# Optimization experiments

Hardware: AMD Instinct MI355X
Metric: run time of the kernel (lower is better)

## Reference

```python
import jax, jax.numpy as jnp
import numpy as np

N = 100000      # nodes
E = 1600000     # edges (avg degree 16)
DIN = 128
DOUT = 128


def setup_inputs() -> dict:
    key = jax.random.key(0)
    k1, k2, k3, k4 = jax.random.split(key, 4)
    x = jax.random.normal(k1, (N, DIN), dtype=jnp.float32)
    edge_index = jax.random.randint(k2, (2, E), 0, N, dtype=jnp.int64)
    # guarantee every node appears at least once as a source row so that
    # degree > 0 everywhere (1/sqrt(0) would be inf, as in the torch code)
    row = edge_index[0].at[:N].set(jnp.arange(N, dtype=jnp.int64))
    edge_index = jnp.stack([row, edge_index[1]])
    W = jax.random.normal(k3, (DOUT, DIN), dtype=jnp.float32) / np.sqrt(DIN)
    b = jax.random.normal(k4, (DOUT,), dtype=jnp.float32) * 0.01
    return {"x": x, "edge_index": edge_index, "W": W, "b": b}


def reference(x, edge_index, W, b):
    # Math identical to: A = dense(add_self_loops(edge_index));
    # D = 1/sqrt(degree(edge_index[0]))  (degree WITHOUT self-loops);
    # out = (D_i * A_ij * D_j) @ (x W^T + b)
    row, col = edge_index[0], edge_index[1]
    deg = jax.ops.segment_sum(jnp.ones(row.shape[0], x.dtype), row, num_segments=N)
    d = jax.lax.rsqrt(deg)                      # [N]
    h = x @ W.T + b                             # [N, DOUT]
    # edge contributions: out[r] += D[r] * D[c] * h[c]  (duplicate edges sum, as to_dense does)
    agg = jax.ops.segment_sum(d[col][:, None] * h[col], row, num_segments=N)
    # self-loop term added for every node: D[i]^2 * h[i]
    out = d[:, None] * agg + (d * d)[:, None] * h
    return out
```

## Files before the change

kernel.cpp:

```cpp
#include <hip/hip_runtime.h>

#define D 128
#define BROWS 1024
#define CAP 17408
#define CHUNK 2048

typedef __attribute__((ext_vector_type(8))) short bf16x8;
typedef __attribute__((ext_vector_type(4))) float f32x4;

__device__ inline unsigned short f2bf(float f) {
    unsigned u = __float_as_uint(f);
    u += 0x7FFFu + ((u >> 16) & 1u);
    return (unsigned short)(u >> 16);
}
__device__ inline float bf2f(unsigned short h) {
    return __uint_as_float((unsigned)h << 16);
}
__device__ inline float bflo(unsigned u) { return __uint_as_float(u << 16); }
__device__ inline float bfhi(unsigned u) { return __uint_as_float(u & 0xFFFF0000u); }

__global__ __launch_bounds__(256) void k_bin(const int* __restrict__ row,
                                             const int* __restrict__ col,
                                             int E, int* __restrict__ gcur,
                                             unsigned* __restrict__ ebuf) {
    __shared__ int lhist[128];
    __shared__ int sc[128];
    __shared__ int gbase[128];
    __shared__ unsigned sstage[CHUNK];
    __shared__ int sdest[CHUNK];
    int t = threadIdx.x;
    int base = blockIdx.x * CHUNK;
    if (t < 128) lhist[t] = 0;
    __syncthreads();
    int b[8], p[8]; unsigned pk[8];
    #pragma unroll
    for (int i = 0; i < 8; ++i) {
        int idx = base + i * 256 + t;
        if (idx < E) {
            int r = row[idx], c = col[idx];
            b[i] = r >> 10;
            pk[i] = ((unsigned)(r & (BROWS - 1)) << 17) | (unsigned)c;
            p[i] = atomicAdd(&lhist[b[i]], 1);
        } else b[i] = -1;
    }
    __syncthreads();
    if (t < 64) {
        int a0 = lhist[2 * t], a1 = lhist[2 * t + 1];
        int s = a0 + a1;
        int incl = s;
        #pragma unroll
        for (int m = 1; m < 64; m <<= 1) {
            int tmp = __shfl_up(incl, m);
            if (t >= m) incl += tmp;
        }
        int excl = incl - s;
        sc[2 * t] = excl;
        sc[2 * t + 1] = excl + a0;
        if (a0 > 0) gbase[2 * t] = atomicAdd(&gcur[2 * t], a0);
        if (a1 > 0) gbase[2 * t + 1] = atomicAdd(&gcur[2 * t + 1], a1);
    }
    __syncthreads();
    #pragma unroll
    for (int i = 0; i < 8; ++i) {
        if (b[i] >= 0) {
            int lidx = sc[b[i]] + p[i];
            int rel = gbase[b[i]] + p[i];
            sstage[lidx] = pk[i];
            sdest[lidx] = (rel < CAP) ? (b[i] * CAP + rel) : -1;
        }
    }
    __syncthreads();
    int total = sc[127] + lhist[127];
    for (int i = t; i < total; i += 256) {
        int d = sdest[i];
        if (d >= 0) ebuf[d] = sstage[i];
    }
}

__global__ __launch_bounds__(1024) void k_group(const int* __restrict__ gcur,
                                                const unsigned* __restrict__ ebuf,
                                                int N, int NBK,
                                                float* __restrict__ dvals,
                                                int* __restrict__ rptr,
                                                int* __restrict__ csr_col) {
    __shared__ unsigned sebuf[CAP];
    __shared__ int lhist[1024];
    __shared__ int wtot[16];
    __shared__ int woff[16];
    __shared__ int sebase;
    int bkt = blockIdx.x, t = threadIdx.x;
    int cnt = gcur[bkt]; if (cnt > CAP) cnt = CAP;
    if (t < 64) {
        int acc = 0;
        for (int i = t; i < bkt; i += 64) {
            int g = gcur[i];
            acc += (g > CAP) ? CAP : g;
        }
        #pragma unroll
        for (int m = 1; m < 64; m <<= 1) acc += __shfl_xor(acc, m);
        if (t == 0) sebase = acc;
    }
    lhist[t] = 0;
    __syncthreads();
    const unsigned* ep = ebuf + (size_t)bkt * CAP;
    for (int i = t; i < cnt; i += 1024) {
        unsigned e = ep[i];
        sebuf[i] = e;
        atomicAdd(&lhist[e >> 17], 1);
    }
    __syncthreads();
    int v = lhist[t];
    int lane = t & 63, wv = t >> 6;
    int incl = v;
    #pragma unroll
    for (int m = 1; m < 64; m <<= 1) {
        int tmp = __shfl_up(incl, m);
        if (lane >= m) incl += tmp;
    }
    if (lane == 63) wtot[wv] = incl;
    __syncthreads();
    if (t < 16) {
        int w = wtot[t];
        int wincl = w;
        #pragma unroll
        for (int m = 1; m < 16; m <<= 1) {
            int tmp = __shfl_up(wincl, m);
            if (t >= m) wincl += tmp;
        }
        woff[t] = wincl - w;
    }
    __syncthreads();
    int excl = woff[wv] + incl - v;
    int ebase = sebase;
    int r = (bkt << 10) + t;
    if (r < N) {
        rptr[r] = ebase + excl;
        dvals[r] = rsqrtf((float)v);
    }
    if (bkt == NBK - 1 && t == 0) rptr[N] = ebase + cnt;
    lhist[t] = excl;
    __syncthreads();
    for (int i = t; i < cnt; i += 1024) {
        unsigned e = sebuf[i];
        int rr = (int)(e >> 17);
        int p = atomicAdd(&lhist[rr], 1);
        csr_col[ebase + p] = (int)(e & 0x1FFFFu);
    }
}

__global__ void k_cast(const float* __restrict__ x, const float* __restrict__ dvals,
                       unsigned short* __restrict__ xs, int total4) {
    int i = blockIdx.x * blockDim.x + threadIdx.x;
    if (i >= total4) return;
    float4 v = ((const float4*)x)[i];
    float d = dvals[i >> 5];
    ushort4 o = make_ushort4(f2bf(d * v.x), f2bf(d * v.y), f2bf(d * v.z), f2bf(d * v.w));
    ((ushort4*)xs)[i] = o;
}

#define ACC8(v) do { \
    a[0] += bflo((v).x); a[1] += bfhi((v).x); \
    a[2] += bflo((v).y); a[3] += bfhi((v).y); \
    a[4] += bflo((v).z); a[5] += bfhi((v).z); \
    a[6] += bflo((v).w); a[7] += bfhi((v).w); } while (0)

__global__ __launch_bounds__(256) void k_rows(const unsigned short* __restrict__ xs,
                                              const int* __restrict__ rptr,
                                              const int* __restrict__ csr_col,
                                              const float* __restrict__ dvals,
                                              float* __restrict__ ssum,
                                              float* __restrict__ y, int N) {
    int wid = (blockIdx.x * blockDim.x + threadIdx.x) >> 6;
    if (wid >= N) return;
    int lane = threadIdx.x & 63;
    int grp = lane >> 4, sl = lane & 15;
    int s = rptr[wid];
    int n = rptr[wid + 1] - s;
    const uint4* xsv = (const uint4*)xs;

    int ccreg = (lane < n) ? csr_col[s + lane] : 0;
    float sd = (lane < n) ? dvals[ccreg] : 0.f;
    uint4 vself = make_uint4(0, 0, 0, 0);
    if (grp == 0) vself = xsv[wid * 16 + sl];

    float a[8] = {0.f, 0.f, 0.f, 0.f, 0.f, 0.f, 0.f, 0.f};
    int nf = (n < 64) ? n : 64;
    for (int k0 = 0; k0 < nf; k0 += 16) {
        int i0 = k0 + grp, i1 = i0 + 4, i2 = i0 + 8, i3 = i0 + 12;
        int cc0 = __shfl(ccreg, i0), cc1 = __shfl(ccreg, i1);
        int cc2 = __shfl(ccreg, i2), cc3 = __shfl(ccreg, i3);
        bool p0 = i0 < nf, p1 = i1 < nf, p2 = i2 < nf, p3 = i3 < nf;
        uint4 v0, v1, v2, v3;
        if (p0) v0 = xsv[cc0 * 16 + sl];
        if (p1) v1 = xsv[cc1 * 16 + sl];
        if (p2) v2 = xsv[cc2 * 16 + sl];
        if (p3) v3 = xsv[cc3 * 16 + sl];
        if (p0) ACC8(v0);
        if (p1) ACC8(v1);
        if (p2) ACC8(v2);
        if (p3) ACC8(v3);
    }
    if (__builtin_expect(n > 64, 0)) {
        for (int idx = 64 + grp; idx < n; idx += 4) {
            int cc = csr_col[s + idx];
            uint4 v = xsv[cc * 16 + sl];
            ACC8(v);
        }
        for (int idx = 64 + lane; idx < n; idx += 64)
            sd += dvals[csr_col[s + idx]];
    }
    if (grp == 0) ACC8(vself);

    #pragma unroll
    for (int j = 0; j < 8; ++j) {
        a[j] += __shfl_xor(a[j], 16);
        a[j] += __shfl_xor(a[j], 32);
    }
    #pragma unroll
    for (int m = 1; m < 64; m <<= 1) sd += __shfl_xor(sd, m);

    float dr = dvals[wid];
    if (grp < 2) {
        float4 o = (grp == 0) ? make_float4(a[0], a[1], a[2], a[3])
                              : make_float4(a[4], a[5], a[6], a[7]);
        o.x *= dr; o.y *= dr; o.z *= dr; o.w *= dr;
        ((float4*)(y + (size_t)wid * D))[sl * 2 + grp] = o;
    }
    if (lane == 0) ssum[wid] = dr * (dr + sd);
}

#define LDSW 136

__global__ __launch_bounds__(256, 2) void k_gemm(const float* __restrict__ W,
                                                 const float* __restrict__ b,
                                                 const float* __restrict__ ssum,
                                                 float* yo, int N) {
    __shared__ unsigned short Whi[128 * LDSW];
    __shared__ unsigned short Wlo[128 * LDSW];
    __shared__ float bs[D];
    int t = threadIdx.x;
    #pragma unroll
    for (int i = 0; i < 16; ++i) {
        int idx4 = i * 256 + t;
        float4 w4 = ((const float4*)W)[idx4];
        int r = idx4 >> 5;
        int c = (idx4 & 31) * 4;
        unsigned short h0 = f2bf(w4.x), h1 = f2bf(w4.y), h2 = f2bf(w4.z), h3 = f2bf(w4.w);
        unsigned short l0 = f2bf(w4.x - bf2f(h0));
        unsigned short l1 = f2bf(w4.y - bf2f(h1));
        unsigned short l2 = f2bf(w4.z - bf2f(h2));
        unsigned short l3 = f2bf(w4.w - bf2f(h3));
        ushort4* ph = (ushort4*)&Whi[r * LDSW + c];
        ushort4* pl = (ushort4*)&Wlo[r * LDSW + c];
        *ph = make_ushort4(h0, h1, h2, h3);
        *pl = make_ushort4(l0, l1, l2, l3);
    }
    if (t < D) bs[t] = b[t];
    __syncthreads();

    int wave = t >> 6, lane = t & 63;
    int quad = lane >> 4, mrow = lane & 15;
    int row_base = blockIdx.x * 128 + wave * 32;

    bf16x8 Ahi[2][4], Alo[2][4];
    #pragma unroll
    for (int s = 0; s < 2; ++s) {
        int grow = row_base + s * 16 + mrow;
        bool ok = grow < N;
        const float* yrow = yo + (size_t)(ok ? grow : 0) * D;
        #pragma unroll
        for (int kk = 0; kk < 4; ++kk) {
            int k0 = kk * 32 + quad * 8;
            float4 f0 = ok ? ((const float4*)(yrow + k0))[0] : make_float4(0, 0, 0, 0);
            float4 f1 = ok ? ((const float4*)(yrow + k0))[1] : make_float4(0, 0, 0, 0);
            float fv[8] = {f0.x, f0.y, f0.z, f0.w, f1.x, f1.y, f1.z, f1.w};
            #pragma unroll
            for (int j = 0; j < 8; ++j) {
                unsigned short h = f2bf(fv[j]);
                Ahi[s][kk][j] = (short)h;
                Alo[s][kk][j] = (short)f2bf(fv[j] - bf2f(h));
            }
        }
    }

    f32x4 acc[2][8];
    #pragma unroll
    for (int s = 0; s < 2; ++s)
        #pragma unroll
        for (int ct = 0; ct < 8; ++ct)
            acc[s][ct] = (f32x4){0.f, 0.f, 0.f, 0.f};

    #pragma unroll
    for (int ct = 0; ct < 8; ++ct) {
        int wrow = ct * 16 + mrow;
        #pragma unroll
        for (int kk = 0; kk < 4; ++kk) {
            int off = wrow * LDSW + kk * 32 + quad * 8;
            bf16x8 Bhi = *(const bf16x8*)&Whi[off];
            bf16x8 Blo = *(const bf16x8*)&Wlo[off];
            #pragma unroll
            for (int s = 0; s < 2; ++s) {
                acc[s][ct] = __builtin_amdgcn_mfma_f32_16x16x32_bf16(Ahi[s][kk], Bhi, acc[s][ct], 0, 0, 0);
                acc[s][ct] = __builtin_amdgcn_mfma_f32_16x16x32_bf16(Alo[s][kk], Bhi, acc[s][ct], 0, 0, 0);
                acc[s][ct] = __builtin_amdgcn_mfma_f32_16x16x32_bf16(Ahi[s][kk], Blo, acc[s][ct], 0, 0, 0);
            }
        }
    }

    #pragma unroll
    for (int s = 0; s < 2; ++s) {
        #pragma unroll
        for (int r = 0; r < 4; ++r) {
            int grow = row_base + s * 16 + quad * 4 + r;
            if (grow < N) {
                float sv = ssum[grow];
                #pragma unroll
                for (int ct = 0; ct < 8; ++ct) {
                    int col = ct * 16 + mrow;
                    yo[(size_t)grow * D + col] = acc[s][ct][r] + sv * bs[col];
                }
            }
        }
    }
}

extern "C" void kernel_launch(void* const* d_in, const int* in_sizes, int n_in,
                              void* d_out, int out_size, void* d_ws, size_t ws_size,
                              hipStream_t stream) {
    const float* x  = (const float*)d_in[0];
    const int*   ei = (const int*)d_in[1];
    const float* W  = (const float*)d_in[2];
    const float* b  = (const float*)d_in[3];
    float* out = (float*)d_out;
    int N = in_sizes[0] / D;
    int E = in_sizes[1] / 2;
    int NBK = (N + BROWS - 1) / BROWS;
    int NCH = (E + CHUNK - 1) / CHUNK;

    int*      gcur    = (int*)d_ws;
    int*      rptr    = gcur + 128;
    float*    dvals   = (float*)(rptr + N + 1);
    float*    ssum    = dvals + N;
    int*      csr_col = (int*)(ssum + N);
    unsigned* ebuf    = (unsigned*)(csr_col + E);
    uintptr_t xs_addr = (uintptr_t)(ebuf + (size_t)NBK * CAP);
    xs_addr = (xs_addr + 15) & ~(uintptr_t)15;
    unsigned short* xs = (unsigned short*)xs_addr;

    hipMemsetAsync(gcur, 0, 128 * sizeof(int), stream);
    k_bin<<<NCH, 256, 0, stream>>>(ei, ei + E, E, gcur, ebuf);
    k_group<<<NBK, 1024, 0, stream>>>(gcur, ebuf, N, NBK, dvals, rptr, csr_col);
    k_cast<<<(N * (D / 4) + 255) / 256, 256, 0, stream>>>(x, dvals, xs, N * (D / 4));
    k_rows<<<(N + 3) / 4, 256, 0, stream>>>(xs, rptr, csr_col, dvals, ssum, out, N);
    k_gemm<<<(N + 127) / 128, 256, 0, stream>>>(W, b, ssum, out, N);
}
```

Before: 276.6 us.

## Fuse row aggregation with GEMM and use finer-grained edge bucketing

Merges the gather-aggregate kernel and the split-bf16 MFMA GEMM into one kernel. Each 1024-thread block aggregates 16 rows into LDS as hi/lo bf16 and immediately multiplies them by W, so the fp32 intermediate is no longer written to and re-read from global memory and a launch is dropped. Bucketing now uses 512-row buckets with larger chunks, and a zeroed sentinel row of xs lets the aggregation load without predication. In exchange, each block reloads and converts W from global/L2, only half the waves do the GEMM, and there are more, smaller grouping blocks.

```diff
diff --git a/kernel.cpp b/kernel.cpp
--- a/kernel.cpp
+++ b/kernel.cpp
@@ -1,9 +1,11 @@
 #include <hip/hip_runtime.h>
 
 #define D 128
-#define BROWS 1024
-#define CAP 17408
-#define CHUNK 2048
+#define BROWS 512
+#define LOGB 9
+#define NBMAX 256
+#define CAP 9216
+#define CHUNK 4096
 
 typedef __attribute__((ext_vector_type(8))) short bf16x8;
 typedef __attribute__((ext_vector_type(4))) float f32x4;
@@ -19,34 +21,34 @@
 __device__ inline float bflo(unsigned u) { return __uint_as_float(u << 16); }
 __device__ inline float bfhi(unsigned u) { return __uint_as_float(u & 0xFFFF0000u); }
 
-__global__ __launch_bounds__(256) void k_bin(const int* __restrict__ row,
+__global__ __launch_bounds__(512) void k_bin(const int* __restrict__ row,
                                              const int* __restrict__ col,
                                              int E, int* __restrict__ gcur,
                                              unsigned* __restrict__ ebuf) {
-    __shared__ int lhist[128];
-    __shared__ int sc[128];
-    __shared__ int gbase[128];
+    __shared__ int lhist[NBMAX];
+    __shared__ int sc[NBMAX];
+    __shared__ int gbase[NBMAX];
     __shared__ unsigned sstage[CHUNK];
     __shared__ int sdest[CHUNK];
     int t = threadIdx.x;
     int base = blockIdx.x * CHUNK;
-    if (t < 128) lhist[t] = 0;
+    if (t < NBMAX) lhist[t] = 0;
     __syncthreads();
     int b[8], p[8]; unsigned pk[8];
     #pragma unroll
     for (int i = 0; i < 8; ++i) {
-        int idx = base + i * 256 + t;
+        int idx = base + i * 512 + t;
         if (idx < E) {
             int r = row[idx], c = col[idx];
-            b[i] = r >> 10;
+            b[i] = r >> LOGB;
             pk[i] = ((unsigned)(r & (BROWS - 1)) << 17) | (unsigned)c;
             p[i] = atomicAdd(&lhist[b[i]], 1);
         } else b[i] = -1;
     }
     __syncthreads();
     if (t < 64) {
-        int a0 = lhist[2 * t], a1 = lhist[2 * t + 1];
-        int s = a0 + a1;
+        int a0 = lhist[4*t], a1 = lhist[4*t+1], a2 = lhist[4*t+2], a3 = lhist[4*t+3];
+        int s = a0 + a1 + a2 + a3;
         int incl = s;
         #pragma unroll
         for (int m = 1; m < 64; m <<= 1) {
@@ -54,10 +56,12 @@
             if (t >= m) incl += tmp;
         }
         int excl = incl - s;
-        sc[2 * t] = excl;
-        sc[2 * t + 1] = excl + a0;
-        if (a0 > 0) gbase[2 * t] = atomicAdd(&gcur[2 * t], a0);
-        if (a1 > 0) gbase[2 * t + 1] = atomicAdd(&gcur[2 * t + 1], a1);
+        sc[4*t] = excl; sc[4*t+1] = excl + a0;
+        sc[4*t+2] = excl + a0 + a1; sc[4*t+3] = excl + a0 + a1 + a2;
+        if (a0 > 0) gbase[4*t]   = atomicAdd(&gcur[4*t],   a0);
+        if (a1 > 0) gbase[4*t+1] = atomicAdd(&gcur[4*t+1], a1);
+        if (a2 > 0) gbase[4*t+2] = atomicAdd(&gcur[4*t+2], a2);
+        if (a3 > 0) gbase[4*t+3] = atomicAdd(&gcur[4*t+3], a3);
     }
     __syncthreads();
     #pragma unroll
@@ -70,8 +74,8 @@
         }
     }
     __syncthreads();
-    int total = sc[127] + lhist[127];
-    for (int i = t; i < total; i += 256) {
+    int total = sc[NBMAX - 1] + lhist[NBMAX - 1];
+    for (int i = t; i < total; i += 512) {
         int d = sdest[i];
         if (d >= 0) ebuf[d] = sstage[i];
     }
@@ -84,9 +88,9 @@
                                                 int* __restrict__ rptr,
                                                 int* __restrict__ csr_col) {
     __shared__ unsigned sebuf[CAP];
-    __shared__ int lhist[1024];
-    __shared__ int wtot[16];
-    __shared__ int woff[16];
+    __shared__ int lhist[BROWS];
+    __shared__ int wtot[8];
+    __shared__ int woff[8];
     __shared__ int sebase;
     int bkt = blockIdx.x, t = threadIdx.x;
     int cnt = gcur[bkt]; if (cnt > CAP) cnt = CAP;
@@ -100,7 +104,7 @@
         for (int m = 1; m < 64; m <<= 1) acc += __shfl_xor(acc, m);
         if (t == 0) sebase = acc;
     }
-    lhist[t] = 0;
+    if (t < BROWS) lhist[t] = 0;
     __syncthreads();
     const unsigned* ep = ebuf + (size_t)bkt * CAP;
     for (int i = t; i < cnt; i += 1024) {
@@ -109,36 +113,41 @@
         atomicAdd(&lhist[e >> 17], 1);
     }
     __syncthreads();
-    int v = lhist[t];
     int lane = t & 63, wv = t >> 6;
-    int incl = v;
-    #pragma unroll
-    for (int m = 1; m < 64; m <<= 1) {
-        int tmp = __shfl_up(incl, m);
-        if (lane >= m) incl += tmp;
-    }
-    if (lane == 63) wtot[wv] = incl;
-    __syncthreads();
-    if (t < 16) {
+    int v = 0, incl = 0;
+    if (t < BROWS) {
+        v = lhist[t];
+        incl = v;
+        #pragma unroll
+        for (int m = 1; m < 64; m <<= 1) {
+            int tmp = __shfl_up(incl, m);
+            if (lane >= m) incl += tmp;
+        }
+        if (lane == 63) wtot[wv] = incl;
+    }
+    __syncthreads();
+    if (t < 8) {
         int w = wtot[t];
         int wincl = w;
         #pragma unroll
-        for (int m = 1; m < 16; m <<= 1) {
+        for (int m = 1; m < 8; m <<= 1) {
             int tmp = __shfl_up(wincl, m);
             if (t >= m) wincl += tmp;
         }
         woff[t] = wincl - w;
     }
     __syncthreads();
-    int excl = woff[wv] + incl - v;
     int ebase = sebase;
-    int r = (bkt << 10) + t;
-    if (r < N) {
-        rptr[r] = ebase + excl;
-        dvals[r] = rsqrtf((float)v);
+    if (t < BROWS) {
+        int excl = woff[wv] + incl - v;
+        int r = (bkt << LOGB) + t;
+        if (r < N) {
+            rptr[r] = ebase + excl;
+            dvals[r] = rsqrtf((float)v);
+        }
+        lhist[t] = excl;
     }
     if (bkt == NBK - 1 && t == 0) rptr[N] = ebase + cnt;
-    lhist[t] = excl;
     __syncthreads();
     for (int i = t; i < cnt; i += 1024) {
         unsigned e = sebuf[i];
@@ -164,53 +173,72 @@
     a[4] += bflo((v).z); a[5] += bfhi((v).z); \
     a[6] += bflo((v).w); a[7] += bfhi((v).w); } while (0)
 
-__global__ __launch_bounds__(256) void k_rows(const unsigned short* __restrict__ xs,
-                                              const int* __restrict__ rptr,
-                                              const int* __restrict__ csr_col,
-                                              const float* __restrict__ dvals,
-                                              float* __restrict__ ssum,
-                                              float* __restrict__ y, int N) {
-    int wid = (blockIdx.x * blockDim.x + threadIdx.x) >> 6;
-    if (wid >= N) return;
-    int lane = threadIdx.x & 63;
-    int grp = lane >> 4, sl = lane & 15;
-    int s = rptr[wid];
-    int n = rptr[wid + 1] - s;
+#define YW 136
+
+__global__ __launch_bounds__(1024, 8) void k_fg(const unsigned short* __restrict__ xs,
+                                                const int* __restrict__ rptr,
+                                                const int* __restrict__ csr_col,
+                                                const float* __restrict__ dvals,
+                                                const float* __restrict__ W,
+                                                const float* __restrict__ b,
+                                                float* __restrict__ out, int N) {
+    __shared__ unsigned short yhi[16][YW];
+    __shared__ unsigned short ylo[16][YW];
+    __shared__ float sval[16];
+    int t = threadIdx.x;
+    int w = t >> 6, lane = t & 63, grp = lane >> 4, sl = lane & 15;
+    int r = blockIdx.x * 16 + w;
     const uint4* xsv = (const uint4*)xs;
 
-    int ccreg = (lane < n) ? csr_col[s + lane] : 0;
-    float sd = (lane < n) ? dvals[ccreg] : 0.f;
-    uint4 vself = make_uint4(0, 0, 0, 0);
-    if (grp == 0) vself = xsv[wid * 16 + sl];
-
     float a[8] = {0.f, 0.f, 0.f, 0.f, 0.f, 0.f, 0.f, 0.f};
-    int nf = (n < 64) ? n : 64;
-    for (int k0 = 0; k0 < nf; k0 += 16) {
-        int i0 = k0 + grp, i1 = i0 + 4, i2 = i0 + 8, i3 = i0 + 12;
-        int cc0 = __shfl(ccreg, i0), cc1 = __shfl(ccreg, i1);
-        int cc2 = __shfl(ccreg, i2), cc3 = __shfl(ccreg, i3);
-        bool p0 = i0 < nf, p1 = i1 < nf, p2 = i2 < nf, p3 = i3 < nf;
-        uint4 v0, v1, v2, v3;
-        if (p0) v0 = xsv[cc0 * 16 + sl];
-        if (p1) v1 = xsv[cc1 * 16 + sl];
-        if (p2) v2 = xsv[cc2 * 16 + sl];
-        if (p3) v3 = xsv[cc3 * 16 + sl];
-        if (p0) ACC8(v0);
-        if (p1) ACC8(v1);
-        if (p2) ACC8(v2);
-        if (p3) ACC8(v3);
-    }
-    if (__builtin_expect(n > 64, 0)) {
-        for (int idx = 64 + grp; idx < n; idx += 4) {
-            int cc = csr_col[s + idx];
-            uint4 v = xsv[cc * 16 + sl];
-            ACC8(v);
-        }
-        for (int idx = 64 + lane; idx < n; idx += 64)
-            sd += dvals[csr_col[s + idx]];
-    }
-    if (grp == 0) ACC8(vself);
-
+    float sd = 0.f;
+    if (r < N) {
+        int sbeg = rptr[r];
+        int n = rptr[r + 1] - sbeg;
+        int cc0 = (lane < n) ? csr_col[sbeg + lane] : -1;
+        int ccreg = (cc0 >= 0) ? cc0 : N;
+        sd = (cc0 >= 0) ? dvals[cc0] : 0.f;
+        uint4 vs = make_uint4(0, 0, 0, 0);
+        if (grp == 0) vs = xsv[(size_t)r * 16 + sl];
+        int nf = (n < 64) ? n : 64;
+        if (nf <= 16) {
+            int c0 = __shfl(ccreg, grp),     c1 = __shfl(ccreg, grp + 4);
+            int c2 = __shfl(ccreg, grp + 8), c3 = __shfl(ccreg, grp + 12);
+            uint4 v0 = xsv[(size_t)c0 * 16 + sl];
+            uint4 v1 = xsv[(size_t)c1 * 16 + sl];
+            uint4 v2 = xsv[(size_t)c2 * 16 + sl];
+            uint4 v3 = xsv[(size_t)c3 * 16 + sl];
+            ACC8(v0); ACC8(v1); ACC8(v2); ACC8(v3);
+        } else {
+            for (int k0 = 0; k0 < nf; k0 += 32) {
+                int i0 = k0 + grp;
+                int c0 = __shfl(ccreg, i0),      c1 = __shfl(ccreg, i0 + 4);
+                int c2 = __shfl(ccreg, i0 + 8),  c3 = __shfl(ccreg, i0 + 12);
+                int c4 = __shfl(ccreg, i0 + 16), c5 = __shfl(ccreg, i0 + 20);
+                int c6 = __shfl(ccreg, i0 + 24), c7 = __shfl(ccreg, i0 + 28);
+                uint4 v0 = xsv[(size_t)c0 * 16 + sl];
+                uint4 v1 = xsv[(size_t)c1 * 16 + sl];
+                uint4 v2 = xsv[(size_t)c2 * 16 + sl];
+                uint4 v3 = xsv[(size_t)c3 * 16 + sl];
+                uint4 v4 = xsv[(size_t)c4 * 16 + sl];
+                uint4 v5 = xsv[(size_t)c5 * 16 + sl];
+                uint4 v6 = xsv[(size_t)c6 * 16 + sl];
+                uint4 v7 = xsv[(size_t)c7 * 16 + sl];
+                ACC8(v0); ACC8(v1); ACC8(v2); ACC8(v3);
+                ACC8(v4); ACC8(v5); ACC8(v6); ACC8(v7);
+            }
+        }
+        if (__builtin_expect(n > 64, 0)) {
+            for (int idx = 64 + grp; idx < n; idx += 4) {
+                int cc = csr_col[sbeg + idx];
+                uint4 v = xsv[(size_t)cc * 16 + sl];
+                ACC8(v);
+            }
+            for (int idx = 64 + lane; idx < n; idx += 64)
+                sd += dvals[csr_col[sbeg + idx]];
+        }
+        if (grp == 0) ACC8(vs);
+    }
     #pragma unroll
     for (int j = 0; j < 8; ++j) {
         a[j] += __shfl_xor(a[j], 16);
@@ -219,107 +247,59 @@
     #pragma unroll
     for (int m = 1; m < 64; m <<= 1) sd += __shfl_xor(sd, m);
 
-    float dr = dvals[wid];
-    if (grp < 2) {
-        float4 o = (grp == 0) ? make_float4(a[0], a[1], a[2], a[3])
-                              : make_float4(a[4], a[5], a[6], a[7]);
-        o.x *= dr; o.y *= dr; o.z *= dr; o.w *= dr;
-        ((float4*)(y + (size_t)wid * D))[sl * 2 + grp] = o;
-    }
-    if (lane == 0) ssum[wid] = dr * (dr + sd);
-}
-
-#define LDSW 136
-
-__global__ __launch_bounds__(256, 2) void k_gemm(const float* __restrict__ W,
-                                                 const float* __restrict__ b,
-                                                 const float* __restrict__ ssum,
-                                                 float* yo, int N) {
-    __shared__ unsigned short Whi[128 * LDSW];
-    __shared__ unsigned short Wlo[128 * LDSW];
-    __shared__ float bs[D];
-    int t = threadIdx.x;
-    #pragma unroll
-    for (int i = 0; i < 16; ++i) {
-        int idx4 = i * 256 + t;
-        float4 w4 = ((const float4*)W)[idx4];
-        int r = idx4 >> 5;
-        int c = (idx4 & 31) * 4;
-        unsigned short h0 = f2bf(w4.x), h1 = f2bf(w4.y), h2 = f2bf(w4.z), h3 = f2bf(w4.w);
-        unsigned short l0 = f2bf(w4.x - bf2f(h0));
-        unsigned short l1 = f2bf(w4.y - bf2f(h1));
-        unsigned short l2 = f2bf(w4.z - bf2f(h2));
-        unsigned short l3 = f2bf(w4.w - bf2f(h3));
-        ushort4* ph = (ushort4*)&Whi[r * LDSW + c];
-        ushort4* pl = (ushort4*)&Wlo[r * LDSW + c];
-        *ph = make_ushort4(h0, h1, h2, h3);
-        *pl = make_ushort4(l0, l1, l2, l3);
-    }
-    if (t < D) bs[t] = b[t];
-    __syncthreads();
-
-    int wave = t >> 6, lane = t & 63;
-    int quad = lane >> 4, mrow = lane & 15;
-    int row_base = blockIdx.x * 128 + wave * 32;
-
-    bf16x8 Ahi[2][4], Alo[2][4];
-    #pragma unroll
-    for (int s = 0; s < 2; ++s) {
-        int grow = row_base + s * 16 + mrow;
-        bool ok = grow < N;
-        const float* yrow = yo + (size_t)(ok ? grow : 0) * D;
+    float dr = (r < N) ? dvals[r] : 0.f;
+    if (grp == 0) {
+        ushort4 h0, h1;
+        h0.x = f2bf(dr * a[0]); h0.y = f2bf(dr * a[1]);
+        h0.z = f2bf(dr * a[2]); h0.w = f2bf(dr * a[3]);
+        h1.x = f2bf(dr * a[4]); h1.y = f2bf(dr * a[5]);
+        h1.z = f2bf(dr * a[6]); h1.w = f2bf(dr * a[7]);
+        ((ushort4*)&yhi[w][sl * 8])[0] = h0;
+        ((ushort4*)&yhi[w][sl * 8])[1] = h1;
+    } else if (grp == 1) {
+        ushort4 l0, l1;
+        float v0 = dr * a[0], v1 = dr * a[1], v2 = dr * a[2], v3 = dr * a[3];
+        float v4 = dr * a[4], v5 = dr * a[5], v6 = dr * a[6], v7 = dr * a[7];
+        l0.x = f2bf(v0 - bf2f(f2bf(v0))); l0.y = f2bf(v1 - bf2f(f2bf(v1)));
+        l0.z = f2bf(v2 - bf2f(f2bf(v2))); l0.w = f2bf(v3 - bf2f(f2bf(v3)));
+        l1.x = f2bf(v4 - bf2f(f2bf(v4))); l1.y = f2bf(v5 - bf2f(f2bf(v5)));
+        l1.z = f2bf(v6 - bf2f(f2bf(v6))); l1.w = f2bf(v7 - bf2f(f2bf(v7)));
+        ((ushort4*)&ylo[w][sl * 8])[0] = l0;
+        ((ushort4*)&ylo[w][sl * 8])[1] = l1;
+    }
+    if (lane == 0) sval[w] = dr * (dr + sd);
+    __syncthreads();
+
+    if (w < 8) {
+        int mrow = lane & 15, quad = lane >> 4;
+        int cw = w * 16 + mrow;
+        const float* wp = W + (size_t)cw * D;
+        f32x4 acc = (f32x4){0.f, 0.f, 0.f, 0.f};
         #pragma unroll
         for (int kk = 0; kk < 4; ++kk) {
             int k0 = kk * 32 + quad * 8;
-            float4 f0 = ok ? ((const float4*)(yrow + k0))[0] : make_float4(0, 0, 0, 0);
-            float4 f1 = ok ? ((const float4*)(yrow + k0))[1] : make_float4(0, 0, 0, 0);
+            bf16x8 Ah = *(const bf16x8*)&yhi[mrow][k0];
+            bf16x8 Al = *(const bf16x8*)&ylo[mrow][k0];
+            float4 f0 = ((const float4*)(wp + k0))[0];
+            float4 f1 = ((const float4*)(wp + k0))[1];
             float fv[8] = {f0.x, f0.y, f0.z, f0.w, f1.x, f1.y, f1.z, f1.w};
+            bf16x8 Bh, Bl;
             #pragma unroll
             for (int j = 0; j < 8; ++j) {
-                unsigned short h = f2bf(fv[j]);
-                Ahi[s][kk][j] = (short)h;
-                Alo[s][kk][j] = (short)f2bf(fv[j] - bf2f(h));
+                unsigned short hh = f2bf(fv[j]);
+                Bh[j] = (short)hh;
+                Bl[j] = (short)f2bf(fv[j] - bf2f(hh));
             }
-        }
-    }
-
-    f32x4 acc[2][8];
-    #pragma unroll
-    for (int s = 0; s < 2; ++s)
-        #pragma unroll
-        for (int ct = 0; ct < 8; ++ct)
-            acc[s][ct] = (f32x4){0.f, 0.f, 0.f, 0.f};
-
-    #pragma unroll
-    for (int ct = 0; ct < 8; ++ct) {
-        int wrow = ct * 16 + mrow;
-        #pragma unroll
-        for (int kk = 0; kk < 4; ++kk) {
-            int off = wrow * LDSW + kk * 32 + quad * 8;
-            bf16x8 Bhi = *(const bf16x8*)&Whi[off];
-            bf16x8 Blo = *(const bf16x8*)&Wlo[off];
-            #pragma unroll
-            for (int s = 0; s < 2; ++s) {
-                acc[s][ct] = __builtin_amdgcn_mfma_f32_16x16x32_bf16(Ahi[s][kk], Bhi, acc[s][ct], 0, 0, 0);
-                acc[s][ct] = __builtin_amdgcn_mfma_f32_16x16x32_bf16(Alo[s][kk], Bhi, acc[s][ct], 0, 0, 0);
-                acc[s][ct] = __builtin_amdgcn_mfma_f32_16x16x32_bf16(Ahi[s][kk], Blo, acc[s][ct], 0, 0, 0);
-            }
-        }
-    }
-
-    #pragma unroll
-    for (int s = 0; s < 2; ++s) {
-        #pragma unroll
-        for (int r = 0; r < 4; ++r) {
-            int grow = row_base + s * 16 + quad * 4 + r;
-            if (grow < N) {
-                float sv = ssum[grow];
-                #pragma unroll
-                for (int ct = 0; ct < 8; ++ct) {
-                    int col = ct * 16 + mrow;
-                    yo[(size_t)grow * D + col] = acc[s][ct][r] + sv * bs[col];
-                }
-            }
+            acc = __builtin_amdgcn_mfma_f32_16x16x32_bf16(Ah, Bh, acc, 0, 0, 0);
+            acc = __builtin_amdgcn_mfma_f32_16x16x32_bf16(Al, Bh, acc, 0, 0, 0);
+            acc = __builtin_amdgcn_mfma_f32_16x16x32_bf16(Ah, Bl, acc, 0, 0, 0);
+        }
+        float bc = b[cw];
+        #pragma unroll
+        for (int q = 0; q < 4; ++q) {
+            int grow = blockIdx.x * 16 + quad * 4 + q;
+            if (grow < N)
+                out[(size_t)grow * D + cw] = acc[q] + sval[quad * 4 + q] * bc;
         }
     }
 }
@@ -334,23 +314,22 @@
     float* out = (float*)d_out;
     int N = in_sizes[0] / D;
     int E = in_sizes[1] / 2;
-    int NBK = (N + BROWS - 1) / BROWS;
+    int NB = (N + BROWS - 1) / BROWS;
     int NCH = (E + CHUNK - 1) / CHUNK;
 
     int*      gcur    = (int*)d_ws;
-    int*      rptr    = gcur + 128;
+    int*      rptr    = gcur + NBMAX;
     float*    dvals   = (float*)(rptr + N + 1);
-    float*    ssum    = dvals + N;
-    int*      csr_col = (int*)(ssum + N);
+    int*      csr_col = (int*)(dvals + N);
     unsigned* ebuf    = (unsigned*)(csr_col + E);
-    uintptr_t xs_addr = (uintptr_t)(ebuf + (size_t)NBK * CAP);
+    uintptr_t xs_addr = (uintptr_t)(ebuf + (size_t)NB * CAP);
     xs_addr = (xs_addr + 15) & ~(uintptr_t)15;
     unsigned short* xs = (unsigned short*)xs_addr;
 
-    hipMemsetAsync(gcur, 0, 128 * sizeof(int), stream);
-    k_bin<<<NCH, 256, 0, stream>>>(ei, ei + E, E, gcur, ebuf);
-    k_group<<<NBK, 1024, 0, stream>>>(gcur, ebuf, N, NBK, dvals, rptr, csr_col);
+    hipMemsetAsync(gcur, 0, NBMAX * sizeof(int), stream);
+    hipMemsetAsync(xs + (size_t)N * D, 0, D * sizeof(unsigned short), stream);
+    k_bin<<<NCH, 512, 0, stream>>>(ei, ei + E, E, gcur, ebuf);
+    k_group<<<NB, 1024, 0, stream>>>(gcur, ebuf, N, NB, dvals, rptr, csr_col);
     k_cast<<<(N * (D / 4) + 255) / 256, 256, 0, stream>>>(x, dvals, xs, N * (D / 4));
-    k_rows<<<(N + 3) / 4, 256, 0, stream>>>(xs, rptr, csr_col, dvals, ssum, out, N);
-    k_gemm<<<(N + 127) / 128, 256, 0, stream>>>(W, b, ssum, out, N);
-}
+    k_fg<<<(N + 15) / 16, 1024, 0, stream>>>(xs, rptr, csr_col, dvals, W, b, out, N);
+}
```

Measured after the change: 328.6 us. +18.8%, slower.
